# Optimization experiments

Hardware: AMD Instinct MI355X
Metric: run time of the kernel (lower is better)

## Reference

```python
import jax, jax.numpy as jnp
import numpy as np

GLM_HIDDEN = 256
K = 3
REL_NUM = K + 1
NUM_BASES = 2
BATCH = 8
SLEN = 2048


def setup_inputs() -> dict:
    key = jax.random.key(0)
    k1, k2, k3, k4, k5 = jax.random.split(key, 5)
    D = GLM_HIDDEN
    x = jax.random.normal(k1, (BATCH, SLEN, D), dtype=jnp.float32)
    # RGCNConv basis decomposition params: W_r = sum_b comp[r,b] * basis[b]
    scale = 1.0 / np.sqrt(D)
    basis = jax.random.normal(k2, (NUM_BASES, D, D), dtype=jnp.float32) * scale
    comp = jax.random.normal(k3, (REL_NUM, NUM_BASES), dtype=jnp.float32)
    root = jax.random.normal(k4, (D, D), dtype=jnp.float32) * scale
    bias = jax.random.normal(k5, (D,), dtype=jnp.float32) * 0.01
    return {"x": x, "comp": comp, "basis": basis, "root": root, "bias": bias}


def reference(x, comp, basis, root, bias):
    B, S, D = x.shape
    R = comp.shape[0]
    Kthr = R - 1
    idx = jnp.arange(S)
    # edge (source s -> target t) has relation min(|t+1 - s|, K); full S x S edge set
    rel = jnp.minimum(jnp.abs((idx[None, :] + 1) - idx[:, None]), Kthr)  # [S(source), S(target)]
    masks = (rel[None, :, :] == jnp.arange(R)[:, None, None]).astype(x.dtype)  # [R,S,T]
    deg = masks.sum(axis=1)  # [R,T] in-degree per relation (PyG aggr='mean')
    inv_deg = jnp.where(deg > 0, 1.0 / deg, 0.0)
    A = masks * inv_deg[:, None, :]  # normalized adjacency per relation [R,S,T]
    # basis-decomposed relation weights
    W = jnp.einsum('rb,bio->rio', comp, basis)  # [R,D,D]
    # aggregate then transform: out[b,t] = sum_r (mean_{s in N_r(t)} x[b,s]) @ W_r
    agg = jnp.einsum('rst,bsi->brti', A, x)  # [B,R,S,D]
    out = jnp.einsum('brti,rio->bto', agg, W)
    out = out + jnp.einsum('bsi,io->bso', x, root) + bias
    return out
```

## Files before the change

### kernel.cpp

```cpp
#include <hip/hip_runtime.h>

#define D 256
#define S 2048
#define B 8
#define DSQ (D * D)
#define INV3 (1.0f / 2043.0f)

typedef __bf16 bf16x8 __attribute__((ext_vector_type(8)));
typedef float f32x4 __attribute__((ext_vector_type(4)));

__device__ __forceinline__ unsigned short f2bf(float f) {
    union { float f; unsigned int u; } v; v.f = f;
    unsigned int u = v.u;
    u += 0x7fffu + ((u >> 16) & 1u);
    return (unsigned short)(u >> 16);
}

__device__ __forceinline__ void gl2lds16(const void* g, void* l) {
    __builtin_amdgcn_global_load_lds(
        (const __attribute__((address_space(1))) void*)g,
        (__attribute__((address_space(3))) void*)l, 16, 0, 0);
}

__global__ __launch_bounds__(256) void k_prep(const float* __restrict__ x,
                                              unsigned short* __restrict__ xh,
                                              float* __restrict__ part) {
    int b = blockIdx.x, chunk = blockIdx.y;
    int tid = threadIdx.x;
    int rg = tid >> 6;
    int c4 = (tid & 63) << 2;
    __shared__ float ps[4][D];
    int row0 = chunk * 32 + rg * 8;
    const float4* xb = (const float4*)(x + ((size_t)b * S + row0) * D + c4);
    ushort4* dst = (ushort4*)(xh + ((size_t)(1 + b * S + row0)) * D + c4);
    float4 s = {0.f, 0.f, 0.f, 0.f};
    #pragma unroll
    for (int i = 0; i < 8; ++i) {
        float4 v = xb[(size_t)i * 64];
        ushort4 o;
        o.x = f2bf(v.x); o.y = f2bf(v.y); o.z = f2bf(v.z); o.w = f2bf(v.w);
        dst[(size_t)i * 64] = o;
        s.x += v.x; s.y += v.y; s.z += v.z; s.w += v.w;
    }
    *(float4*)&ps[rg][c4] = s;
    __syncthreads();
    part[((size_t)(b * 64 + chunk)) * D + tid] =
        ps[0][tid] + ps[1][tid] + ps[2][tid] + ps[3][tid];
}

__global__ __launch_bounds__(256) void k_weights(
        const float* __restrict__ basis, const float* __restrict__ comp,
        const float* __restrict__ root, const float* __restrict__ bias,
        const float* __restrict__ part, const float* __restrict__ x,
        unsigned short* __restrict__ Cbs, float* __restrict__ Tb,
        float* __restrict__ out) {
    int blk = blockIdx.x;
    int tid = threadIdx.x;

    if (blk < 160) {
        int step = blk >> 2, q = blk & 3;
        int ji = step >> 3, kc = step & 7;
        int n = tid;
        float a0 = (ji == 2) ? 1.f : 0.f;
        float a1 = (ji == 1 || ji == 3) ? 0.5f : 0.f;
        float a2 = (ji == 0 || ji == 4) ? 0.5f : 0.f;
        float ar = (ji == 1) ? 1.f : 0.f;
        float cb0 = a0 * comp[0] + a1 * comp[2] + a2 * comp[4] - INV3 * comp[6];
        float cb1 = a0 * comp[1] + a1 * comp[3] + a2 * comp[5] - INV3 * comp[7];
        unsigned short buf[8];
        #pragma unroll
        for (int kk = 0; kk < 8; ++kk) {
            int i = kc * 32 + q * 8 + kk;
            float v = cb0 * basis[i * D + n] + cb1 * basis[DSQ + i * D + n]
                    + ar * root[i * D + n];
            buf[kk] = f2bf(v);
        }
        *(uint4*)(Cbs + ((size_t)step * 256 + n) * 32 + q * 8) = *(uint4*)buf;
    } else if (blk < 168) {
        int b = blk - 160;
        __shared__ float tot[D];
        float t = 0.f;
        #pragma unroll 8
        for (int c = 0; c < 64; ++c) t += part[((size_t)(b * 64 + c)) * D + tid];
        tot[tid] = t;
        __syncthreads();
        int o = tid;
        float c30 = comp[6], c31 = comp[7];
        float acc = 0.f;
        #pragma unroll 4
        for (int k = 0; k < D; ++k)
            acc += tot[k] * (c30 * basis[k * D + o] + c31 * basis[DSQ + k * D + o]);
        Tb[b * D + o] = bias[o] + acc * INV3;
    } else {
        int r = blk - 168;
        const int tl[4] = {0, S - 3, S - 2, S - 1};
        int t = tl[r & 3], b = r >> 2;
        __shared__ float z0[D], z1[D], xr[D];
        const float* xb = x + (size_t)b * S * D;
        int i = tid;
        float tot = 0.f;
        #pragma unroll 8
        for (int c = 0; c < 64; ++c) tot += part[((size_t)(b * 64 + c)) * D + i];
        float x_t = xb[(size_t)t * D + i];
        float v0 = (t + 1 < S) ? xb[(size_t)(t + 1) * D + i] : 0.f;
        float d1 = 1.f + ((t + 2 < S) ? 1.f : 0.f);
        float v1 = (x_t + ((t + 2 < S) ? xb[(size_t)(t + 2) * D + i] : 0.f)) / d1;
        float s2 = ((t - 1 >= 0) ? xb[(size_t)(t - 1) * D + i] : 0.f)
                 + ((t + 3 < S) ? xb[(size_t)(t + 3) * D + i] : 0.f);
        int d2i = ((t - 1 >= 0) ? 1 : 0) + ((t + 3 < S) ? 1 : 0);
        float v2 = d2i ? s2 / (float)d2i : 0.f;
        float wsum = 0.f;
        for (int s = t - 1; s <= t + 3; ++s)
            if (s >= 0 && s < S) wsum += xb[(size_t)s * D + i];
        int d3i = ((t - 1 > 0) ? (t - 1) : 0) + ((S - 4 - t > 0) ? (S - 4 - t) : 0);
        float v3 = d3i ? (tot - wsum) / (float)d3i : 0.f;
        z0[i] = comp[0] * v0 + comp[2] * v1 + comp[4] * v2 + comp[6] * v3;
        z1[i] = comp[1] * v0 + comp[3] * v1 + comp[5] * v2 + comp[7] * v3;
        xr[i] = x_t;
        __syncthreads();
        int o = tid;
        float acc = 0.f;
        #pragma unroll 8
        for (int k = 0; k < D; ++k) {
            acc += z0[k] * basis[k * D + o] + z1[k] * basis[DSQ + k * D + o]
                 + xr[k] * root[k * D + o];
        }
        out[(((size_t)b * S + t) << 8) + o] = acc + bias[o];
    }
}

__global__ __launch_bounds__(128) void k_bulk_mfma(
        const unsigned short* __restrict__ xh,
        const unsigned short* __restrict__ Cbs,
        const float* __restrict__ Tb,
        float* __restrict__ out) {
    __shared__ __align__(16) unsigned short xs[132 * 256];
    const int tid  = threadIdx.x;
    const int lane = tid & 63;
    const int w    = tid >> 6;
    const int mblk = blockIdx.x;
    const int nblk = blockIdx.y;
    const int b  = mblk >> 4;
    const int t0 = (mblk & 15) << 7;
    const size_t rowbase = (size_t)b * S + t0;

    #pragma unroll
    for (int q = 0; q < 33; ++q) {
        int F = (q * 128 + tid) * 16;
        int r = F >> 9;
        int c16 = (F >> 4) & 31;
        int gc = (c16 & 24) | ((c16 ^ r) & 7);
        gl2lds16((const char*)xh + ((rowbase + r) << 9) + (gc << 4), (char*)xs + F);
    }
    __syncthreads();

    const int rlo = lane & 15, q4 = lane >> 4;
    #define BFRAG(st, nt) (*(const bf16x8*)(Cbs + \
        (((size_t)(st) * 256 + nblk * 64 + (nt) * 16 + rlo) << 5) + (q4 << 3)))

    f32x4 acc[4][4] = {};
    bf16x8 bb[3][4];
    #pragma unroll
    for (int nt = 0; nt < 4; ++nt) { bb[0][nt] = BFRAG(0, nt); bb[1][nt] = BFRAG(1, nt); }

    #pragma unroll
    for (int step = 0; step < 40; ++step) {
        const int cur = step % 3;
        const int pfs = (step + 2 < 40) ? step + 2 : 39;
        const int pbuf = (step + 2) % 3;
        #pragma unroll
        for (int nt = 0; nt < 4; ++nt) bb[pbuf][nt] = BFRAG(pfs, nt);

        const int ji = step >> 3, kc = step & 7;
        bf16x8 a[4];
        #pragma unroll
        for (int mt = 0; mt < 4; ++mt) {
            int r = w * 64 + mt * 16 + rlo + ji;
            int cc = kc * 4 + q4;
            int c16 = (cc & 24) | ((cc ^ r) & 7);
            a[mt] = *(const bf16x8*)((const char*)xs + (r << 9) + (c16 << 4));
        }
        #pragma unroll
        for (int mt = 0; mt < 4; ++mt)
            #pragma unroll
            for (int nt = 0; nt < 4; ++nt)
                acc[mt][nt] = __builtin_amdgcn_mfma_f32_16x16x32_bf16(a[mt], bb[cur][nt], acc[mt][nt], 0, 0, 0);
    }
    #undef BFRAG

    const int col = lane & 15, rq = (lane >> 4) << 2;
    #pragma unroll
    for (int nt = 0; nt < 4; ++nt) {
        int n = nblk * 64 + nt * 16 + col;
        float tb = Tb[b * D + n];
        #pragma unroll
        for (int mt = 0; mt < 4; ++mt) {
            #pragma unroll
            for (int i = 0; i < 4; ++i) {
                int t = t0 + w * 64 + mt * 16 + rq + i;
                if (t >= 1 && t <= S - 4)
                    out[(((size_t)b * S + t) << 8) + n] = acc[mt][nt][i] + tb;
            }
        }
    }
}


extern "C" void kernel_launch(void* const* d_in, const int* in_sizes, int n_in,
                              void* d_out, int out_size, void* d_ws, size_t ws_size,
                              hipStream_t stream) {
    const float* x     = (const float*)d_in[0];
    const float* comp  = (const float*)d_in[1];
    const float* basis = (const float*)d_in[2];
    const float* root  = (const float*)d_in[3];
    const float* bias  = (const float*)d_in[4];
    float* out = (float*)d_out;

    char* ws = (char*)d_ws;
    float* part         = (float*)(ws);
    float* Tb           = (float*)(ws + 524288);
    unsigned short* Cbs = (unsigned short*)(ws + 532480);
    unsigned short* xh  = (unsigned short*)(ws + 1187840);

    k_prep     <<<dim3(B, 64), 256, 0, stream>>>(x, xh, part);
    k_weights  <<<200,         256, 0, stream>>>(basis, comp, root, bias, part, x, Cbs, Tb, out);
    k_bulk_mfma<<<dim3(128, 4), 128, 0, stream>>>(xh, Cbs, Tb, out);
}
```

Measured before the change: 122.0 us.

## Fuse three kernels into one cooperative kernel with grid-wide syncs

Merges the prep, weight-building and MFMA GEMM kernels into a single cooperative launch of 512 blocks of 128 threads, separated by grid.sync barriers. Each block does the bf16 conversion and partial sums for 32 rows, and some blocks also build the combined weights, before moving on to the tail rows and the GEMM tile. This removes two kernel launch gaps. In exchange it adds grid-barrier cost, needs all 512 blocks to be resident at once with about 66KB of LDS each, and halves the thread count in the weight and tail phases.

```diff
diff --git a/kernel.cpp b/kernel.cpp
--- a/kernel.cpp
+++ b/kernel.cpp
@@ -1,4 +1,7 @@
 #include <hip/hip_runtime.h>
+#include <hip/hip_cooperative_groups.h>
+
+namespace cg = cooperative_groups;
 
 #define D 256
 #define S 2048
@@ -22,184 +25,202 @@
         (__attribute__((address_space(3))) void*)l, 16, 0, 0);
 }
 
-__global__ __launch_bounds__(256) void k_prep(const float* __restrict__ x,
-                                              unsigned short* __restrict__ xh,
-                                              float* __restrict__ part) {
-    int b = blockIdx.x, chunk = blockIdx.y;
-    int tid = threadIdx.x;
-    int rg = tid >> 6;
-    int c4 = (tid & 63) << 2;
-    __shared__ float ps[4][D];
-    int row0 = chunk * 32 + rg * 8;
-    const float4* xb = (const float4*)(x + ((size_t)b * S + row0) * D + c4);
-    ushort4* dst = (ushort4*)(xh + ((size_t)(1 + b * S + row0)) * D + c4);
-    float4 s = {0.f, 0.f, 0.f, 0.f};
-    #pragma unroll
-    for (int i = 0; i < 8; ++i) {
-        float4 v = xb[(size_t)i * 64];
-        ushort4 o;
-        o.x = f2bf(v.x); o.y = f2bf(v.y); o.z = f2bf(v.z); o.w = f2bf(v.w);
-        dst[(size_t)i * 64] = o;
-        s.x += v.x; s.y += v.y; s.z += v.z; s.w += v.w;
-    }
-    *(float4*)&ps[rg][c4] = s;
-    __syncthreads();
-    part[((size_t)(b * 64 + chunk)) * D + tid] =
-        ps[0][tid] + ps[1][tid] + ps[2][tid] + ps[3][tid];
-}
-
-__global__ __launch_bounds__(256) void k_weights(
-        const float* __restrict__ basis, const float* __restrict__ comp,
-        const float* __restrict__ root, const float* __restrict__ bias,
-        const float* __restrict__ part, const float* __restrict__ x,
+__global__ __launch_bounds__(128) void k_fused(
+        const float* __restrict__ x, const float* __restrict__ comp,
+        const float* __restrict__ basis, const float* __restrict__ root,
+        const float* __restrict__ bias,
+        unsigned short* __restrict__ xh, float* __restrict__ part,
         unsigned short* __restrict__ Cbs, float* __restrict__ Tb,
         float* __restrict__ out) {
-    int blk = blockIdx.x;
-    int tid = threadIdx.x;
-
-    if (blk < 160) {
-        int step = blk >> 2, q = blk & 3;
-        int ji = step >> 3, kc = step & 7;
-        int n = tid;
-        float a0 = (ji == 2) ? 1.f : 0.f;
-        float a1 = (ji == 1 || ji == 3) ? 0.5f : 0.f;
-        float a2 = (ji == 0 || ji == 4) ? 0.5f : 0.f;
-        float ar = (ji == 1) ? 1.f : 0.f;
-        float cb0 = a0 * comp[0] + a1 * comp[2] + a2 * comp[4] - INV3 * comp[6];
-        float cb1 = a0 * comp[1] + a1 * comp[3] + a2 * comp[5] - INV3 * comp[7];
-        unsigned short buf[8];
-        #pragma unroll
-        for (int kk = 0; kk < 8; ++kk) {
-            int i = kc * 32 + q * 8 + kk;
-            float v = cb0 * basis[i * D + n] + cb1 * basis[DSQ + i * D + n]
-                    + ar * root[i * D + n];
-            buf[kk] = f2bf(v);
-        }
-        *(uint4*)(Cbs + ((size_t)step * 256 + n) * 32 + q * 8) = *(uint4*)buf;
-    } else if (blk < 168) {
+    __shared__ __align__(16) char smem[67584];
+    const int blk = blockIdx.x;
+    const int tid = threadIdx.x;
+    cg::grid_group grid = cg::this_grid();
+
+    {
+        float* ps = (float*)smem;
+        int rg = tid >> 6;
+        int c4 = (tid & 63) << 2;
+        int row0 = blk * 32 + rg * 16;
+        const float4* xb = (const float4*)(x + (size_t)row0 * D + c4);
+        ushort4* dst = (ushort4*)(xh + (size_t)(1 + row0) * D + c4);
+        float4 s = {0.f, 0.f, 0.f, 0.f};
+        #pragma unroll
+        for (int i = 0; i < 16; ++i) {
+            float4 v = xb[(size_t)i * 64];
+            ushort4 o;
+            o.x = f2bf(v.x); o.y = f2bf(v.y); o.z = f2bf(v.z); o.w = f2bf(v.w);
+            dst[(size_t)i * 64] = o;
+            s.x += v.x; s.y += v.y; s.z += v.z; s.w += v.w;
+        }
+        *(float4*)&ps[rg * D + c4] = s;
+
+        if (blk < 160) {
+            int step = blk >> 2, q = blk & 3;
+            int ji = step >> 3, kc = step & 7;
+            float a0 = (ji == 2) ? 1.f : 0.f;
+            float a1 = (ji == 1 || ji == 3) ? 0.5f : 0.f;
+            float a2 = (ji == 0 || ji == 4) ? 0.5f : 0.f;
+            float ar = (ji == 1) ? 1.f : 0.f;
+            float cb0 = a0 * comp[0] + a1 * comp[2] + a2 * comp[4] - INV3 * comp[6];
+            float cb1 = a0 * comp[1] + a1 * comp[3] + a2 * comp[5] - INV3 * comp[7];
+            #pragma unroll
+            for (int h = 0; h < 2; ++h) {
+                int n = h * 128 + tid;
+                unsigned short buf[8];
+                #pragma unroll
+                for (int kk = 0; kk < 8; ++kk) {
+                    int i = kc * 32 + q * 8 + kk;
+                    buf[kk] = f2bf(cb0 * basis[i * D + n] + cb1 * basis[DSQ + i * D + n]
+                                   + ar * root[i * D + n]);
+                }
+                *(uint4*)(Cbs + ((size_t)step * 256 + n) * 32 + q * 8) = *(uint4*)buf;
+            }
+        }
+        __syncthreads();
+        if (tid < 64)
+            *(float4*)&part[(size_t)blk * D + tid * 4] =
+                *(float4*)&ps[tid * 4] + *(float4*)&ps[D + tid * 4];
+    }
+
+    grid.sync();
+
+    if (blk >= 160 && blk < 168) {
         int b = blk - 160;
-        __shared__ float tot[D];
-        float t = 0.f;
-        #pragma unroll 8
-        for (int c = 0; c < 64; ++c) t += part[((size_t)(b * 64 + c)) * D + tid];
-        tot[tid] = t;
-        __syncthreads();
-        int o = tid;
+        float* tot = (float*)smem;
+        #pragma unroll
+        for (int h = 0; h < 2; ++h) {
+            int ch = h * 128 + tid;
+            float t = 0.f;
+            #pragma unroll 8
+            for (int c = 0; c < 64; ++c) t += part[(size_t)(b * 64 + c) * D + ch];
+            tot[ch] = t;
+        }
+        __syncthreads();
         float c30 = comp[6], c31 = comp[7];
-        float acc = 0.f;
-        #pragma unroll 4
-        for (int k = 0; k < D; ++k)
-            acc += tot[k] * (c30 * basis[k * D + o] + c31 * basis[DSQ + k * D + o]);
-        Tb[b * D + o] = bias[o] + acc * INV3;
-    } else {
+        #pragma unroll
+        for (int h = 0; h < 2; ++h) {
+            int o = h * 128 + tid;
+            float acc = 0.f;
+            #pragma unroll 4
+            for (int k = 0; k < D; ++k)
+                acc += tot[k] * (c30 * basis[k * D + o] + c31 * basis[DSQ + k * D + o]);
+            Tb[b * D + o] = bias[o] + acc * INV3;
+        }
+    } else if (blk >= 168 && blk < 200) {
         int r = blk - 168;
         const int tl[4] = {0, S - 3, S - 2, S - 1};
         int t = tl[r & 3], b = r >> 2;
-        __shared__ float z0[D], z1[D], xr[D];
+        float* z0 = (float*)smem;
+        float* z1 = z0 + D;
+        float* xr = z1 + D;
         const float* xb = x + (size_t)b * S * D;
-        int i = tid;
-        float tot = 0.f;
-        #pragma unroll 8
-        for (int c = 0; c < 64; ++c) tot += part[((size_t)(b * 64 + c)) * D + i];
-        float x_t = xb[(size_t)t * D + i];
-        float v0 = (t + 1 < S) ? xb[(size_t)(t + 1) * D + i] : 0.f;
-        float d1 = 1.f + ((t + 2 < S) ? 1.f : 0.f);
-        float v1 = (x_t + ((t + 2 < S) ? xb[(size_t)(t + 2) * D + i] : 0.f)) / d1;
-        float s2 = ((t - 1 >= 0) ? xb[(size_t)(t - 1) * D + i] : 0.f)
-                 + ((t + 3 < S) ? xb[(size_t)(t + 3) * D + i] : 0.f);
-        int d2i = ((t - 1 >= 0) ? 1 : 0) + ((t + 3 < S) ? 1 : 0);
-        float v2 = d2i ? s2 / (float)d2i : 0.f;
-        float wsum = 0.f;
-        for (int s = t - 1; s <= t + 3; ++s)
-            if (s >= 0 && s < S) wsum += xb[(size_t)s * D + i];
-        int d3i = ((t - 1 > 0) ? (t - 1) : 0) + ((S - 4 - t > 0) ? (S - 4 - t) : 0);
-        float v3 = d3i ? (tot - wsum) / (float)d3i : 0.f;
-        z0[i] = comp[0] * v0 + comp[2] * v1 + comp[4] * v2 + comp[6] * v3;
-        z1[i] = comp[1] * v0 + comp[3] * v1 + comp[5] * v2 + comp[7] * v3;
-        xr[i] = x_t;
-        __syncthreads();
-        int o = tid;
-        float acc = 0.f;
-        #pragma unroll 8
-        for (int k = 0; k < D; ++k) {
-            acc += z0[k] * basis[k * D + o] + z1[k] * basis[DSQ + k * D + o]
-                 + xr[k] * root[k * D + o];
-        }
-        out[(((size_t)b * S + t) << 8) + o] = acc + bias[o];
+        #pragma unroll
+        for (int h = 0; h < 2; ++h) {
+            int i = h * 128 + tid;
+            float tot = 0.f;
+            #pragma unroll 8
+            for (int c = 0; c < 64; ++c) tot += part[(size_t)(b * 64 + c) * D + i];
+            float x_t = xb[(size_t)t * D + i];
+            float v0 = (t + 1 < S) ? xb[(size_t)(t + 1) * D + i] : 0.f;
+            float d1 = 1.f + ((t + 2 < S) ? 1.f : 0.f);
+            float v1 = (x_t + ((t + 2 < S) ? xb[(size_t)(t + 2) * D + i] : 0.f)) / d1;
+            float s2 = ((t - 1 >= 0) ? xb[(size_t)(t - 1) * D + i] : 0.f)
+                     + ((t + 3 < S) ? xb[(size_t)(t + 3) * D + i] : 0.f);
+            int d2i = ((t - 1 >= 0) ? 1 : 0) + ((t + 3 < S) ? 1 : 0);
+            float v2 = d2i ? s2 / (float)d2i : 0.f;
+            float wsum = 0.f;
+            for (int s = t - 1; s <= t + 3; ++s)
+                if (s >= 0 && s < S) wsum += xb[(size_t)s * D + i];
+            int d3i = ((t - 1 > 0) ? (t - 1) : 0) + ((S - 4 - t > 0) ? (S - 4 - t) : 0);
+            float v3 = d3i ? (tot - wsum) / (float)d3i : 0.f;
+            z0[i] = comp[0] * v0 + comp[2] * v1 + comp[4] * v2 + comp[6] * v3;
+            z1[i] = comp[1] * v0 + comp[3] * v1 + comp[5] * v2 + comp[7] * v3;
+            xr[i] = x_t;
+        }
+        __syncthreads();
+        #pragma unroll
+        for (int h = 0; h < 2; ++h) {
+            int o = h * 128 + tid;
+            float acc = 0.f;
+            #pragma unroll 8
+            for (int k = 0; k < D; ++k)
+                acc += z0[k] * basis[k * D + o] + z1[k] * basis[DSQ + k * D + o]
+                     + xr[k] * root[k * D + o];
+            out[(((size_t)b * S + t) << 8) + o] = acc + bias[o];
+        }
     }
-}
-
-__global__ __launch_bounds__(128) void k_bulk_mfma(
-        const unsigned short* __restrict__ xh,
-        const unsigned short* __restrict__ Cbs,
-        const float* __restrict__ Tb,
-        float* __restrict__ out) {
-    __shared__ __align__(16) unsigned short xs[132 * 256];
-    const int tid  = threadIdx.x;
-    const int lane = tid & 63;
-    const int w    = tid >> 6;
-    const int mblk = blockIdx.x;
-    const int nblk = blockIdx.y;
-    const int b  = mblk >> 4;
-    const int t0 = (mblk & 15) << 7;
-    const size_t rowbase = (size_t)b * S + t0;
-
-    #pragma unroll
-    for (int q = 0; q < 33; ++q) {
-        int F = (q * 128 + tid) * 16;
-        int r = F >> 9;
-        int c16 = (F >> 4) & 31;
-        int gc = (c16 & 24) | ((c16 ^ r) & 7);
-        gl2lds16((const char*)xh + ((rowbase + r) << 9) + (gc << 4), (char*)xs + F);
-    }
-    __syncthreads();
-
-    const int rlo = lane & 15, q4 = lane >> 4;
-    #define BFRAG(st, nt) (*(const bf16x8*)(Cbs + \
-        (((size_t)(st) * 256 + nblk * 64 + (nt) * 16 + rlo) << 5) + (q4 << 3)))
-
-    f32x4 acc[4][4] = {};
-    bf16x8 bb[3][4];
-    #pragma unroll
-    for (int nt = 0; nt < 4; ++nt) { bb[0][nt] = BFRAG(0, nt); bb[1][nt] = BFRAG(1, nt); }
-
-    #pragma unroll
-    for (int step = 0; step < 40; ++step) {
-        const int cur = step % 3;
-        const int pfs = (step + 2 < 40) ? step + 2 : 39;
-        const int pbuf = (step + 2) % 3;
-        #pragma unroll
-        for (int nt = 0; nt < 4; ++nt) bb[pbuf][nt] = BFRAG(pfs, nt);
-
-        const int ji = step >> 3, kc = step & 7;
-        bf16x8 a[4];
-        #pragma unroll
-        for (int mt = 0; mt < 4; ++mt) {
-            int r = w * 64 + mt * 16 + rlo + ji;
-            int cc = kc * 4 + q4;
-            int c16 = (cc & 24) | ((cc ^ r) & 7);
-            a[mt] = *(const bf16x8*)((const char*)xs + (r << 9) + (c16 << 4));
-        }
-        #pragma unroll
-        for (int mt = 0; mt < 4; ++mt)
-            #pragma unroll
-            for (int nt = 0; nt < 4; ++nt)
-                acc[mt][nt] = __builtin_amdgcn_mfma_f32_16x16x32_bf16(a[mt], bb[cur][nt], acc[mt][nt], 0, 0, 0);
-    }
-    #undef BFRAG
-
-    const int col = lane & 15, rq = (lane >> 4) << 2;
-    #pragma unroll
-    for (int nt = 0; nt < 4; ++nt) {
-        int n = nblk * 64 + nt * 16 + col;
-        float tb = Tb[b * D + n];
-        #pragma unroll
-        for (int mt = 0; mt < 4; ++mt) {
-            #pragma unroll
-            for (int i = 0; i < 4; ++i) {
-                int t = t0 + w * 64 + mt * 16 + rq + i;
-                if (t >= 1 && t <= S - 4)
-                    out[(((size_t)b * S + t) << 8) + n] = acc[mt][nt][i] + tb;
+
+    grid.sync();
+
+    {
+        unsigned short* xs = (unsigned short*)smem;
+        const int lane = tid & 63;
+        const int w    = tid >> 6;
+        const int nblk = blk & 3;
+        const int mblk = blk >> 2;
+        const int b  = mblk >> 4;
+        const int t0 = (mblk & 15) << 7;
+        const size_t rowbase = (size_t)b * S + t0;
+
+        __syncthreads();
+        #pragma unroll
+        for (int q = 0; q < 33; ++q) {
+            int F = (q * 128 + tid) * 16;
+            int r = F >> 9;
+            int c16 = (F >> 4) & 31;
+            int gc = (c16 & 24) | ((c16 ^ r) & 7);
+            gl2lds16((const char*)xh + ((rowbase + r) << 9) + (gc << 4), (char*)xs + F);
+        }
+        __syncthreads();
+
+        const int rlo = lane & 15, q4 = lane >> 4;
+        #define BFRAG(st, nt) (*(const bf16x8*)(Cbs + \
+            (((size_t)(st) * 256 + nblk * 64 + (nt) * 16 + rlo) << 5) + (q4 << 3)))
+
+        f32x4 acc[4][4] = {};
+        bf16x8 bb[3][4];
+        #pragma unroll
+        for (int nt = 0; nt < 4; ++nt) { bb[0][nt] = BFRAG(0, nt); bb[1][nt] = BFRAG(1, nt); }
+
+        #pragma unroll
+        for (int step = 0; step < 40; ++step) {
+            const int cur = step % 3;
+            const int pfs = (step + 2 < 40) ? step + 2 : 39;
+            const int pbuf = (step + 2) % 3;
+            #pragma unroll
+            for (int nt = 0; nt < 4; ++nt) bb[pbuf][nt] = BFRAG(pfs, nt);
+
+            const int ji = step >> 3, kc = step & 7;
+            bf16x8 a[4];
+            #pragma unroll
+            for (int mt = 0; mt < 4; ++mt) {
+                int r = w * 64 + mt * 16 + rlo + ji;
+                int cc = kc * 4 + q4;
+                int c16 = (cc & 24) | ((cc ^ r) & 7);
+                a[mt] = *(const bf16x8*)((const char*)xs + (r << 9) + (c16 << 4));
+            }
+            #pragma unroll
+            for (int mt = 0; mt < 4; ++mt)
+                #pragma unroll
+                for (int nt = 0; nt < 4; ++nt)
+                    acc[mt][nt] = __builtin_amdgcn_mfma_f32_16x16x32_bf16(a[mt], bb[cur][nt], acc[mt][nt], 0, 0, 0);
+        }
+        #undef BFRAG
+
+        const int col = lane & 15, rq = (lane >> 4) << 2;
+        #pragma unroll
+        for (int nt = 0; nt < 4; ++nt) {
+            int n = nblk * 64 + nt * 16 + col;
+            float tb = Tb[b * D + n];
+            #pragma unroll
+            for (int mt = 0; mt < 4; ++mt) {
+                #pragma unroll
+                for (int i = 0; i < 4; ++i) {
+                    int t = t0 + w * 64 + mt * 16 + rq + i;
+                    if (t >= 1 && t <= S - 4)
+                        out[(((size_t)b * S + t) << 8) + n] = acc[mt][nt][i] + tb;
+                }
             }
         }
     }
@@ -222,7 +243,7 @@
     unsigned short* Cbs = (unsigned short*)(ws + 532480);
     unsigned short* xh  = (unsigned short*)(ws + 1187840);
 
-    k_prep     <<<dim3(B, 64), 256, 0, stream>>>(x, xh, part);
-    k_weights  <<<200,         256, 0, stream>>>(basis, comp, root, bias, part, x, Cbs, Tb, out);
-    k_bulk_mfma<<<dim3(128, 4), 128, 0, stream>>>(xh, Cbs, Tb, out);
-}
+    void* args[] = {(void*)&x, (void*)&comp, (void*)&basis, (void*)&root, (void*)&bias,
+                    (void*)&xh, (void*)&part, (void*)&Cbs, (void*)&Tb, (void*)&out};
+    hipLaunchCooperativeKernel((void*)k_fused, dim3(512), dim3(128), args, 0, stream);
+}
```

Measured after the change: 271.3 us. 2.22x slower.

## Move weight packing into prep kernel and widen GEMM blocks to 2x2 waves

Applied to the files above, without the earlier changes.

Folds the combined-weight (Cbs) bf16 packing into the first 160 blocks of the prep kernel, so k_weights only computes the bias terms and boundary rows. The main MFMA kernel now uses 256-thread blocks arranged as a 2x2 wave grid covering 128 rows by 128 columns. Each staged x tile is therefore reused across twice as many output columns, and the grid shrinks from 128x4 to 128x2. It also double-buffers the A fragments read from LDS and deepens B-fragment prefetch to 3 steps, which costs extra registers and may lower occupancy.

```diff
diff --git a/kernel.cpp b/kernel.cpp
--- a/kernel.cpp
+++ b/kernel.cpp
@@ -23,13 +23,18 @@
 }
 
 __global__ __launch_bounds__(256) void k_prep(const float* __restrict__ x,
+                                              const float* __restrict__ comp,
+                                              const float* __restrict__ basis,
+                                              const float* __restrict__ root,
                                               unsigned short* __restrict__ xh,
-                                              float* __restrict__ part) {
-    int b = blockIdx.x, chunk = blockIdx.y;
+                                              float* __restrict__ part,
+                                              unsigned short* __restrict__ Cbs) {
+    int blk = blockIdx.x;
     int tid = threadIdx.x;
+    int b = blk >> 6, chunk = blk & 63;
+    __shared__ float ps[4][D];
     int rg = tid >> 6;
     int c4 = (tid & 63) << 2;
-    __shared__ float ps[4][D];
     int row0 = chunk * 32 + rg * 8;
     const float4* xb = (const float4*)(x + ((size_t)b * S + row0) * D + c4);
     ushort4* dst = (ushort4*)(xh + ((size_t)(1 + b * S + row0)) * D + c4);
@@ -43,19 +48,6 @@
         s.x += v.x; s.y += v.y; s.z += v.z; s.w += v.w;
     }
     *(float4*)&ps[rg][c4] = s;
-    __syncthreads();
-    part[((size_t)(b * 64 + chunk)) * D + tid] =
-        ps[0][tid] + ps[1][tid] + ps[2][tid] + ps[3][tid];
-}
-
-__global__ __launch_bounds__(256) void k_weights(
-        const float* __restrict__ basis, const float* __restrict__ comp,
-        const float* __restrict__ root, const float* __restrict__ bias,
-        const float* __restrict__ part, const float* __restrict__ x,
-        unsigned short* __restrict__ Cbs, float* __restrict__ Tb,
-        float* __restrict__ out) {
-    int blk = blockIdx.x;
-    int tid = threadIdx.x;
 
     if (blk < 160) {
         int step = blk >> 2, q = blk & 3;
@@ -71,17 +63,32 @@
         #pragma unroll
         for (int kk = 0; kk < 8; ++kk) {
             int i = kc * 32 + q * 8 + kk;
-            float v = cb0 * basis[i * D + n] + cb1 * basis[DSQ + i * D + n]
-                    + ar * root[i * D + n];
-            buf[kk] = f2bf(v);
+            buf[kk] = f2bf(cb0 * basis[i * D + n] + cb1 * basis[DSQ + i * D + n]
+                           + ar * root[i * D + n]);
         }
         *(uint4*)(Cbs + ((size_t)step * 256 + n) * 32 + q * 8) = *(uint4*)buf;
-    } else if (blk < 168) {
-        int b = blk - 160;
+    }
+    __syncthreads();
+    if (tid < 64)
+        *(float4*)&part[(size_t)blk * D + tid * 4] =
+            *(float4*)&ps[0][tid * 4] + *(float4*)&ps[1][tid * 4] +
+            *(float4*)&ps[2][tid * 4] + *(float4*)&ps[3][tid * 4];
+}
+
+__global__ __launch_bounds__(256) void k_weights(
+        const float* __restrict__ basis, const float* __restrict__ comp,
+        const float* __restrict__ root, const float* __restrict__ bias,
+        const float* __restrict__ part, const float* __restrict__ x,
+        float* __restrict__ Tb, float* __restrict__ out) {
+    int blk = blockIdx.x;
+    int tid = threadIdx.x;
+
+    if (blk < 8) {
+        int b = blk;
         __shared__ float tot[D];
         float t = 0.f;
         #pragma unroll 8
-        for (int c = 0; c < 64; ++c) t += part[((size_t)(b * 64 + c)) * D + tid];
+        for (int c = 0; c < 64; ++c) t += part[(size_t)(b * 64 + c) * D + tid];
         tot[tid] = t;
         __syncthreads();
         int o = tid;
@@ -92,7 +99,7 @@
             acc += tot[k] * (c30 * basis[k * D + o] + c31 * basis[DSQ + k * D + o]);
         Tb[b * D + o] = bias[o] + acc * INV3;
     } else {
-        int r = blk - 168;
+        int r = blk - 8;
         const int tl[4] = {0, S - 3, S - 2, S - 1};
         int t = tl[r & 3], b = r >> 2;
         __shared__ float z0[D], z1[D], xr[D];
@@ -100,7 +107,7 @@
         int i = tid;
         float tot = 0.f;
         #pragma unroll 8
-        for (int c = 0; c < 64; ++c) tot += part[((size_t)(b * 64 + c)) * D + i];
+        for (int c = 0; c < 64; ++c) tot += part[(size_t)(b * 64 + c) * D + i];
         float x_t = xb[(size_t)t * D + i];
         float v0 = (t + 1 < S) ? xb[(size_t)(t + 1) * D + i] : 0.f;
         float d1 = 1.f + ((t + 2 < S) ? 1.f : 0.f);
@@ -121,15 +128,14 @@
         int o = tid;
         float acc = 0.f;
         #pragma unroll 8
-        for (int k = 0; k < D; ++k) {
+        for (int k = 0; k < D; ++k)
             acc += z0[k] * basis[k * D + o] + z1[k] * basis[DSQ + k * D + o]
                  + xr[k] * root[k * D + o];
-        }
         out[(((size_t)b * S + t) << 8) + o] = acc + bias[o];
     }
 }
 
-__global__ __launch_bounds__(128) void k_bulk_mfma(
+__global__ __launch_bounds__(256) void k_bulk(
         const unsigned short* __restrict__ xh,
         const unsigned short* __restrict__ Cbs,
         const float* __restrict__ Tb,
@@ -138,6 +144,8 @@
     const int tid  = threadIdx.x;
     const int lane = tid & 63;
     const int w    = tid >> 6;
+    const int wm   = w & 1;
+    const int wn   = w >> 1;
     const int mblk = blockIdx.x;
     const int nblk = blockIdx.y;
     const int b  = mblk >> 4;
@@ -145,59 +153,72 @@
     const size_t rowbase = (size_t)b * S + t0;
 
     #pragma unroll
-    for (int q = 0; q < 33; ++q) {
-        int F = (q * 128 + tid) * 16;
+    for (int q = 0; q < 16; ++q) {
+        int F = (q * 256 + tid) * 16;
         int r = F >> 9;
         int c16 = (F >> 4) & 31;
         int gc = (c16 & 24) | ((c16 ^ r) & 7);
         gl2lds16((const char*)xh + ((rowbase + r) << 9) + (gc << 4), (char*)xs + F);
     }
+    if (tid < 128) {
+        int F = (4096 + tid) * 16;
+        int r = F >> 9;
+        int c16 = (F >> 4) & 31;
+        int gc = (c16 & 24) | ((c16 ^ r) & 7);
+        gl2lds16((const char*)xh + ((rowbase + r) << 9) + (gc << 4), (char*)xs + F);
+    }
     __syncthreads();
 
     const int rlo = lane & 15, q4 = lane >> 4;
+    const int nstrip = nblk * 128 + wn * 64;
+    const int mbase  = wm * 64;
+
     #define BFRAG(st, nt) (*(const bf16x8*)(Cbs + \
-        (((size_t)(st) * 256 + nblk * 64 + (nt) * 16 + rlo) << 5) + (q4 << 3)))
+        (((size_t)(st) * 256 + nstrip + (nt) * 16 + rlo) << 5) + (q4 << 3)))
+    #define AFRAG(st, mt) (*(const bf16x8*)((const char*)xs + \
+        (((mbase + (mt) * 16 + rlo + ((st) >> 3))) << 9) + \
+        (((((st) & 7) * 4 + q4) & 24 | ((((st) & 7) * 4 + q4) ^ \
+          (mbase + (mt) * 16 + rlo + ((st) >> 3))) & 7) << 4)))
 
     f32x4 acc[4][4] = {};
-    bf16x8 bb[3][4];
-    #pragma unroll
-    for (int nt = 0; nt < 4; ++nt) { bb[0][nt] = BFRAG(0, nt); bb[1][nt] = BFRAG(1, nt); }
+    bf16x8 bb[4][4];
+    bf16x8 aa[2][4];
+    #pragma unroll
+    for (int nt = 0; nt < 4; ++nt) {
+        bb[0][nt] = BFRAG(0, nt); bb[1][nt] = BFRAG(1, nt); bb[2][nt] = BFRAG(2, nt);
+    }
+    #pragma unroll
+    for (int mt = 0; mt < 4; ++mt) aa[0][mt] = AFRAG(0, mt);
 
     #pragma unroll
     for (int step = 0; step < 40; ++step) {
-        const int cur = step % 3;
-        const int pfs = (step + 2 < 40) ? step + 2 : 39;
-        const int pbuf = (step + 2) % 3;
-        #pragma unroll
-        for (int nt = 0; nt < 4; ++nt) bb[pbuf][nt] = BFRAG(pfs, nt);
-
-        const int ji = step >> 3, kc = step & 7;
-        bf16x8 a[4];
-        #pragma unroll
-        for (int mt = 0; mt < 4; ++mt) {
-            int r = w * 64 + mt * 16 + rlo + ji;
-            int cc = kc * 4 + q4;
-            int c16 = (cc & 24) | ((cc ^ r) & 7);
-            a[mt] = *(const bf16x8*)((const char*)xs + (r << 9) + (c16 << 4));
-        }
+        const int pfB = (step + 3 < 40) ? step + 3 : 39;
+        #pragma unroll
+        for (int nt = 0; nt < 4; ++nt) bb[(step + 3) & 3][nt] = BFRAG(pfB, nt);
+        const int pfA = (step + 1 < 40) ? step + 1 : 39;
+        #pragma unroll
+        for (int mt = 0; mt < 4; ++mt) aa[(step + 1) & 1][mt] = AFRAG(pfA, mt);
+
         #pragma unroll
         for (int mt = 0; mt < 4; ++mt)
             #pragma unroll
             for (int nt = 0; nt < 4; ++nt)
-                acc[mt][nt] = __builtin_amdgcn_mfma_f32_16x16x32_bf16(a[mt], bb[cur][nt], acc[mt][nt], 0, 0, 0);
+                acc[mt][nt] = __builtin_amdgcn_mfma_f32_16x16x32_bf16(
+                    aa[step & 1][mt], bb[step & 3][nt], acc[mt][nt], 0, 0, 0);
     }
     #undef BFRAG
+    #undef AFRAG
 
     const int col = lane & 15, rq = (lane >> 4) << 2;
     #pragma unroll
     for (int nt = 0; nt < 4; ++nt) {
-        int n = nblk * 64 + nt * 16 + col;
+        int n = nstrip + nt * 16 + col;
         float tb = Tb[b * D + n];
         #pragma unroll
         for (int mt = 0; mt < 4; ++mt) {
             #pragma unroll
             for (int i = 0; i < 4; ++i) {
-                int t = t0 + w * 64 + mt * 16 + rq + i;
+                int t = t0 + mbase + mt * 16 + rq + i;
                 if (t >= 1 && t <= S - 4)
                     out[(((size_t)b * S + t) << 8) + n] = acc[mt][nt][i] + tb;
             }
@@ -222,7 +243,7 @@
     unsigned short* Cbs = (unsigned short*)(ws + 532480);
     unsigned short* xh  = (unsigned short*)(ws + 1187840);
 
-    k_prep     <<<dim3(B, 64), 256, 0, stream>>>(x, xh, part);
-    k_weights  <<<200,         256, 0, stream>>>(basis, comp, root, bias, part, x, Cbs, Tb, out);
-    k_bulk_mfma<<<dim3(128, 4), 128, 0, stream>>>(xh, Cbs, Tb, out);
-}
+    k_prep   <<<512,          256, 0, stream>>>(x, comp, basis, root, xh, part, Cbs);
+    k_weights<<<40,           256, 0, stream>>>(basis, comp, root, bias, part, x, Tb, out);
+    k_bulk   <<<dim3(128, 2), 256, 0, stream>>>(xh, Cbs, Tb, out);
+}
```

Measured after the change: 118.9 us. 1.03x faster.
